# Kernel optimization log

Hardware: AMD Instinct MI355X
Metric: run time of the kernel (lower is better)

The kernel has to match this reference:

```python
import jax, jax.numpy as jnp
import numpy as np

E = 1024
M = 6
GH = 256
FR = 16  # FiLM bottleneck r = max(16, E//64)


def setup_inputs() -> dict:
    key = jax.random.key(0)
    ks = jax.random.split(key, 32)
    n = lambda k, shape, std=0.02: jax.random.normal(k, shape, dtype=jnp.float32) * std
    inp = {
        "x": jax.random.normal(ks[0], (4, 2048, E), dtype=jnp.float32),
        # gate MLP E->GH->M
        "gw1": n(ks[1], (E, GH)), "gb1": jnp.zeros((GH,), jnp.float32),
        "gw2": n(ks[2], (GH, M)), "gb2": jnp.zeros((M,), jnp.float32),
        "ebias": jnp.zeros((M,), jnp.float32),
        "pm_alpha": jnp.float32(0.5),
        # expert 0: DoubleMLP E->2E->E
        "dfc_w": n(ks[3], (E, 2 * E)), "dfc_b": jnp.zeros((2 * E,), jnp.float32),
        "dproj_w": n(ks[4], (2 * E, E)), "dproj_b": jnp.zeros((E,), jnp.float32),
        # expert 1: SingleMLP E->E->E
        "sfc_w": n(ks[5], (E, E)), "sfc_b": jnp.zeros((E,), jnp.float32),
        "sproj_w": n(ks[6], (E, E)), "sproj_b": jnp.zeros((E,), jnp.float32),
        # expert 2: rank-2 perceptron
        "p2_w": n(ks[7], (2, E)), "p2_v": n(ks[8], (2, E)),
        "p2_alpha": jnp.ones((2,), jnp.float32), "p2_b": jnp.zeros((2,), jnp.float32),
        "p2_bias": jnp.zeros((E,), jnp.float32),
        # expert 3: rank-4 perceptron
        "p4_w": n(ks[9], (4, E)), "p4_v": n(ks[10], (4, E)),
        "p4_alpha": jnp.ones((4,), jnp.float32), "p4_b": jnp.zeros((4,), jnp.float32),
        "p4_bias": jnp.zeros((E,), jnp.float32),
        # expert 4: ReGLU1D
        "rg_u": n(ks[11], (E,)), "rg_a": jnp.ones((E,), jnp.float32),
        "rg_b": jnp.zeros((1,), jnp.float32), "rg_bias": jnp.zeros((E,), jnp.float32),
        # expert 5: FiLM E->FR->2E
        "fl_dw": n(ks[12], (E, FR)), "fl_db": jnp.zeros((FR,), jnp.float32),
        "fl_uw": n(ks[13], (FR, 2 * E)), "fl_ub": jnp.zeros((2 * E,), jnp.float32),
    }
    return inp


def _gelu(x):
    return jax.nn.gelu(x, approximate=False)  # torch nn.GELU default (erf)


def _rank_n(x, w, v, alpha, b, biasvec):
    # y = biasvec + sum_i alpha_i * gelu(<w_i,x> + b_i) * v_i
    s = jnp.einsum("bse,ne->bsn", x, w) + b
    g = _gelu(s)
    return jnp.einsum("bsn,ne->bse", alpha * g, v) + biasvec


def reference(x, gw1, gb1, gw2, gb2, ebias, pm_alpha,
              dfc_w, dfc_b, dproj_w, dproj_b,
              sfc_w, sfc_b, sproj_w, sproj_b,
              p2_w, p2_v, p2_alpha, p2_b, p2_bias,
              p4_w, p4_v, p4_alpha, p4_b, p4_bias,
              rg_u, rg_a, rg_b, rg_bias,
              fl_dw, fl_db, fl_uw, fl_ub):
    # gate logits [B,S,M]; tau=1.0
    gl = _gelu(x @ gw1 + gb1) @ gw2 + gb2 + ebias
    pi = jax.nn.softmax(gl, axis=-1)
    # top_k=1 sparse weights: mask to top-1 then renormalize
    _, topi = jax.lax.top_k(pi, 1)
    mask = jax.nn.one_hot(topi[..., 0], M, dtype=pi.dtype)
    w = pi * mask
    w = w / (jnp.sum(w, axis=-1, keepdims=True) + 1e-9)

    # experts (dropout = identity in eval)
    o0 = _gelu(x @ dfc_w + dfc_b) @ dproj_w + dproj_b            # DoubleMLP
    o1 = _gelu(x @ sfc_w + sfc_b) @ sproj_w + sproj_b            # SingleMLP
    o2 = _rank_n(x, p2_w, p2_v, p2_alpha, p2_b, p2_bias)          # perc2
    o3 = _rank_n(x, p4_w, p4_v, p4_alpha, p4_b, p4_bias)          # perc4
    s = x @ rg_u + rg_b[0]                                        # ReGLU1D
    o4 = jax.nn.sigmoid(s)[..., None] * (x * rg_a) + rg_bias
    t = _gelu(x @ fl_dw + fl_db)                                  # FiLM
    gb = t @ fl_uw + fl_ub
    gamma, beta = jnp.split(gb, 2, axis=-1)
    o5 = gamma * x + beta

    all_out = jnp.stack([o0, o1, o2, o3, o4, o5], axis=-1)        # [B,S,E,M]
    mixed = jnp.sum(all_out * w[..., None, :], axis=-1)
    return pm_alpha * mixed
```

## Files before the change

kernel.cpp:

```cpp
#include <hip/hip_runtime.h>
#include <math.h>


#define E 1024
#define GH 256
#define NEXP 6
#define NTOK 8192
#define NCH 24

typedef __attribute__((ext_vector_type(8))) short bf16x8;
typedef __attribute__((ext_vector_type(4))) float f32x4;

__device__ __forceinline__ float gelu_erf(float v) {
    return 0.5f * v * (1.0f + erff(v * 0.70710678118654752440f));
}

__device__ __forceinline__ unsigned short f2bf(float f) {
    union { float f; unsigned u; } c; c.f = f;
    unsigned u = c.u;
    u += 0x7fffu + ((u >> 16) & 1u);
    return (unsigned short)(u >> 16);
}

__device__ __forceinline__ float bf2f(unsigned short h) {
    union { unsigned u; float f; } c; c.u = ((unsigned)h) << 16;
    return c.f;
}

__device__ __forceinline__ int ldso(int row, int q) {
    return row * 32 + ((q ^ ((row >> 1) & 3)) << 3);
}

__device__ __forceinline__ void glds16(const void* g, void* l) {
    __builtin_amdgcn_global_load_lds(
        (const __attribute__((address_space(1))) void*)g,
        (__attribute__((address_space(3))) void*)l, 16, 0, 0);
}

__global__ __launch_bounds__(256)
void prep_kernel(const float* __restrict__ x, unsigned short* __restrict__ xh,
                 unsigned short* __restrict__ xl,
                 const float* __restrict__ gw1, unsigned short* __restrict__ w1cat,
                 const float* __restrict__ p2_w, const float* __restrict__ p4_w,
                 const float* __restrict__ rg_u, const float* __restrict__ fl_dw,
                 unsigned short* __restrict__ w1cheap,
                 const float* __restrict__ dfc_w, unsigned short* __restrict__ dfc_wt,
                 const float* __restrict__ dproj_w, unsigned short* __restrict__ dpj_wt,
                 const float* __restrict__ sfc_w, unsigned short* __restrict__ sfc_wt,
                 const float* __restrict__ sproj_w, unsigned short* __restrict__ spj_wt) {
    __shared__ float tile[32][33];
    const int tid = threadIdx.x;
    const int tx = tid & 31, ty = tid >> 5;
    int b = blockIdx.x;
    if (b < 2048) {
        const int n4 = NTOK * E / 4;
        for (int i = b * 256 + tid; i < n4; i += 2048 * 256) {
            float4 v = reinterpret_cast<const float4*>(x)[i];
            ushort4 h, l;
            h.x = f2bf(v.x); l.x = f2bf(v.x - bf2f(h.x));
            h.y = f2bf(v.y); l.y = f2bf(v.y - bf2f(h.y));
            h.z = f2bf(v.z); l.z = f2bf(v.z - bf2f(h.z));
            h.w = f2bf(v.w); l.w = f2bf(v.w - bf2f(h.w));
            reinterpret_cast<ushort4*>(xh)[i] = h;
            reinterpret_cast<ushort4*>(xl)[i] = l;
        }
        return;
    }
    b -= 2048;
    if (b < 256) {
        const int c0 = (b & 7) * 32, r0 = (b >> 3) * 32;
#pragma unroll
        for (int i = 0; i < 4; ++i)
            tile[ty + i * 8][tx] = gw1[(size_t)(r0 + ty + i * 8) * GH + c0 + tx];
        __syncthreads();
#pragma unroll
        for (int i = 0; i < 4; ++i) {
            float v = tile[tx][ty + i * 8];
            unsigned short h = f2bf(v);
            size_t row = (size_t)(c0 + ty + i * 8) * 2048;
            w1cat[row + r0 + tx] = h;
            w1cat[row + 1024 + r0 + tx] = f2bf(v - bf2f(h));
        }
        return;
    }
    b -= 256;
    if (b < 64) {
        const int r = b;
        const int k4 = tid * 4;
        float4 v = {0.f, 0.f, 0.f, 0.f};
        if (r < 2)       v = *reinterpret_cast<const float4*>(&p2_w[r * E + k4]);
        else if (r < 6)  v = *reinterpret_cast<const float4*>(&p4_w[(r - 2) * E + k4]);
        else if (r == 6) v = *reinterpret_cast<const float4*>(&rg_u[k4]);
        else if (r < 23) {
            const int j = r - 7;
            v.x = fl_dw[(k4 + 0) * 16 + j];
            v.y = fl_dw[(k4 + 1) * 16 + j];
            v.z = fl_dw[(k4 + 2) * 16 + j];
            v.w = fl_dw[(k4 + 3) * 16 + j];
        }
        ushort4 h, l;
        h.x = f2bf(v.x); l.x = f2bf(v.x - bf2f(h.x));
        h.y = f2bf(v.y); l.y = f2bf(v.y - bf2f(h.y));
        h.z = f2bf(v.z); l.z = f2bf(v.z - bf2f(h.z));
        h.w = f2bf(v.w); l.w = f2bf(v.w - bf2f(h.w));
        *reinterpret_cast<ushort4*>(&w1cheap[r * 2048 + k4]) = h;
        *reinterpret_cast<ushort4*>(&w1cheap[r * 2048 + 1024 + k4]) = l;
        return;
    }
    b -= 64;
    const float* src; unsigned short* dst; int R, C, nbx;
    if (b < 2048)      { src = dfc_w;   dst = dfc_wt; R = 1024; C = 2048; nbx = 64; }
    else if (b < 4096) { src = dproj_w; dst = dpj_wt; R = 2048; C = 1024; nbx = 32; b -= 2048; }
    else if (b < 5120) { src = sfc_w;   dst = sfc_wt; R = 1024; C = 1024; nbx = 32; b -= 4096; }
    else               { src = sproj_w; dst = spj_wt; R = 1024; C = 1024; nbx = 32; b -= 5120; }
    const int c0 = (b % nbx) * 32, r0 = (b / nbx) * 32;
#pragma unroll
    for (int i = 0; i < 4; ++i)
        tile[ty + i * 8][tx] = src[(size_t)(r0 + ty + i * 8) * C + c0 + tx];
    __syncthreads();
#pragma unroll
    for (int i = 0; i < 4; ++i)
        dst[(size_t)(c0 + ty + i * 8) * R + r0 + tx] = f2bf(tile[tx][ty + i * 8]);
}

__global__ __launch_bounds__(256)
void gate_partial_kernel(const unsigned short* __restrict__ xh,
                         const unsigned short* __restrict__ xl,
                         const unsigned short* __restrict__ w1cat,
                         const unsigned short* __restrict__ w1cheap,
                         float* __restrict__ hp,
                         float* __restrict__ cdot) {
    __shared__ __align__(16) unsigned short As[2][128 * 64];
    __shared__ __align__(16) unsigned short Bs[2][128 * 64];
    const int tid = threadIdx.x;
    const int bid = blockIdx.x;
    const int xcd = bid & 7, slot = bid >> 3;
    const int nx = slot & 1;
    const int strip = xcd * 32 + (slot >> 1);
    const int m = strip >> 2, c2 = strip & 3;
    const int z = c2 & 1, h = c2 >> 1;
    const int t0 = m * 128, n0 = nx * 128;
    const unsigned short* A = z ? xl : xh;
    float* hpz = hp + (size_t)c2 * ((size_t)NTOK * GH);
    float* cd  = cdot + (size_t)c2 * ((size_t)NTOK * NCH);

    const int lane = tid & 63, wv = tid >> 6;
    const int wr = wv >> 1, wc = wv & 1;
    const int lm = lane & 15, q = lane >> 4;
    const int r0 = tid >> 2, gsl = tid & 3;
    const int g = gsl ^ ((r0 >> 1) & 3);
    const int lbase = wv * 512;

    const unsigned short* pa0 = A + (size_t)(t0 + r0) * E + g * 8;
    const unsigned short* pa1 = A + (size_t)(t0 + 64 + r0) * E + g * 8;
    const unsigned short* pb0 = w1cat + (size_t)(n0 + r0) * 2048 + h * 1024 + g * 8;
    const unsigned short* pb1 = w1cat + (size_t)(n0 + 64 + r0) * 2048 + h * 1024 + g * 8;
    const unsigned short* pcw = w1cheap + (size_t)(nx * 16 + lm) * 2048 + h * 1024 + q * 8;

    f32x4 acc[4][4];
#pragma unroll
    for (int s = 0; s < 4; ++s)
#pragma unroll
        for (int t = 0; t < 4; ++t) acc[s][t] = (f32x4){0.f, 0.f, 0.f, 0.f};
    f32x4 accC[2];
    accC[0] = (f32x4){0.f, 0.f, 0.f, 0.f};
    accC[1] = (f32x4){0.f, 0.f, 0.f, 0.f};

    glds16(pa0, &As[0][lbase]);
    glds16(pa1, &As[0][2048 + lbase]);
    glds16(pa0 + 32, &As[0][4096 + lbase]);
    glds16(pa1 + 32, &As[0][4096 + 2048 + lbase]);
    glds16(pb0, &Bs[0][lbase]);
    glds16(pb1, &Bs[0][2048 + lbase]);
    glds16(pb0 + 32, &Bs[0][4096 + lbase]);
    glds16(pb1 + 32, &Bs[0][4096 + 2048 + lbase]);
    bf16x8 cf0 = *(const bf16x8*)pcw;
    bf16x8 cf1 = *(const bf16x8*)(pcw + 32);

    int cur = 0;
    for (int k0 = 0;; k0 += 64) {
        __syncthreads();
        const int kn = k0 + 64;
        bf16x8 cf0n, cf1n;
        if (kn < 1024) {
            glds16(pa0 + kn, &As[cur ^ 1][lbase]);
            glds16(pa1 + kn, &As[cur ^ 1][2048 + lbase]);
            glds16(pa0 + kn + 32, &As[cur ^ 1][4096 + lbase]);
            glds16(pa1 + kn + 32, &As[cur ^ 1][4096 + 2048 + lbase]);
            glds16(pb0 + kn, &Bs[cur ^ 1][lbase]);
            glds16(pb1 + kn, &Bs[cur ^ 1][2048 + lbase]);
            glds16(pb0 + kn + 32, &Bs[cur ^ 1][4096 + lbase]);
            glds16(pb1 + kn + 32, &Bs[cur ^ 1][4096 + 2048 + lbase]);
            cf0n = *(const bf16x8*)(pcw + kn);
            cf1n = *(const bf16x8*)(pcw + kn + 32);
        }
#pragma unroll
        for (int sub = 0; sub < 2; ++sub) {
            const int off = sub * 4096;
            bf16x8 af[4], bfr[4];
#pragma unroll
            for (int s = 0; s < 4; ++s) af[s] = *(const bf16x8*)&As[cur][off + ldso(wr * 64 + s * 16 + lm, q)];
#pragma unroll
            for (int t = 0; t < 4; ++t) bfr[t] = *(const bf16x8*)&Bs[cur][off + ldso(wc * 64 + t * 16 + lm, q)];
#pragma unroll
            for (int s = 0; s < 4; ++s)
#pragma unroll
                for (int t = 0; t < 4; ++t)
                    acc[s][t] = __builtin_amdgcn_mfma_f32_16x16x32_bf16(af[s], bfr[t], acc[s][t], 0, 0, 0);
            bf16x8 cf = sub ? cf1 : cf0;
            bf16x8 ac0 = wc ? af[2] : af[0];
            bf16x8 ac1 = wc ? af[3] : af[1];
            accC[0] = __builtin_amdgcn_mfma_f32_16x16x32_bf16(ac0, cf, accC[0], 0, 0, 0);
            accC[1] = __builtin_amdgcn_mfma_f32_16x16x32_bf16(ac1, cf, accC[1], 0, 0, 0);
        }
        if (kn >= 1024) break;
        cf0 = cf0n; cf1 = cf1n; cur ^= 1;
    }
#pragma unroll
    for (int s = 0; s < 4; ++s)
#pragma unroll
        for (int t = 0; t < 4; ++t)
#pragma unroll
            for (int rg = 0; rg < 4; ++rg) {
                int rl = wr * 64 + s * 16 + q * 4 + rg;
                int c  = wc * 64 + t * 16 + lm;
                hpz[(size_t)(t0 + rl) * GH + n0 + c] = acc[s][t][rg];
            }
    const int cc = nx * 16 + lm;
    if (cc < NCH) {
#pragma unroll
        for (int i = 0; i < 2; ++i)
#pragma unroll
            for (int rg = 0; rg < 4; ++rg) {
                int rl = wr * 64 + wc * 32 + i * 16 + q * 4 + rg;
                cd[(size_t)(t0 + rl) * NCH + cc] = accC[i][rg];
            }
    }
}

__global__ __launch_bounds__(256)
void gate_finalize_kernel(const float* __restrict__ hp,
                          const float* __restrict__ gb1, const float* __restrict__ gw2,
                          const float* __restrict__ gb2, const float* __restrict__ ebias,
                          const float* __restrict__ pm_alpha,
                          const float* __restrict__ cdot,
                          const float* __restrict__ p2_alpha, const float* __restrict__ p2_b,
                          const float* __restrict__ p4_alpha, const float* __restrict__ p4_b,
                          const float* __restrict__ rg_b, const float* __restrict__ fl_db,
                          float* __restrict__ scale, int* __restrict__ counts,
                          int* __restrict__ tlist, int* __restrict__ eid,
                          float* __restrict__ gvec) {
    __shared__ float hs[32][264];
    __shared__ float g2s[GH * NEXP];
    __shared__ int tokexp[32];
    const int tid = threadIdx.x;
    const int t0 = blockIdx.x * 32;
    const size_t HPS = (size_t)NTOK * GH;
    for (int i = tid; i < GH * NEXP; i += 256) g2s[i] = gw2[i];
#pragma unroll
    for (int i = 0; i < 8; ++i) {
        int f4 = i * 256 + tid;
        int row = f4 >> 6, c4 = (f4 & 63) * 4;
        size_t base = (size_t)(t0 + row) * GH + c4;
        float4 a = *reinterpret_cast<const float4*>(&hp[base]);
        float4 b = *reinterpret_cast<const float4*>(&hp[HPS + base]);
        float4 c = *reinterpret_cast<const float4*>(&hp[2 * HPS + base]);
        float4 d = *reinterpret_cast<const float4*>(&hp[3 * HPS + base]);
        float4 o;
        o.x = gelu_erf(a.x + b.x + c.x + d.x + gb1[c4 + 0]);
        o.y = gelu_erf(a.y + b.y + c.y + d.y + gb1[c4 + 1]);
        o.z = gelu_erf(a.z + b.z + c.z + d.z + gb1[c4 + 2]);
        o.w = gelu_erf(a.w + b.w + c.w + d.w + gb1[c4 + 3]);
        *reinterpret_cast<float4*>(&hs[row][c4]) = o;
    }
    __syncthreads();
    const int t = tid >> 3, j = tid & 7;
    float p[NEXP] = {0.f, 0.f, 0.f, 0.f, 0.f, 0.f};
#pragma unroll 8
    for (int kk = 0; kk < 32; ++kk) {
        int k = j + kk * 8;
        float hv = hs[t][k];
        const float* gr = &g2s[k * NEXP];
#pragma unroll
        for (int m = 0; m < NEXP; ++m) p[m] += hv * gr[m];
    }
#pragma unroll
    for (int m = 0; m < NEXP; ++m) {
        p[m] += __shfl_xor(p[m], 4, 64);
        p[m] += __shfl_xor(p[m], 2, 64);
        p[m] += __shfl_xor(p[m], 1, 64);
    }
    if (j == 0) {
        float L[NEXP];
#pragma unroll
        for (int m = 0; m < NEXP; ++m) L[m] = p[m] + gb2[m] + ebias[m];
        float mx = L[0]; int am = 0;
#pragma unroll
        for (int m = 1; m < NEXP; ++m) { if (L[m] > mx) { mx = L[m]; am = m; } }
        float S = 0.f;
#pragma unroll
        for (int m = 0; m < NEXP; ++m) S += expf(L[m] - mx);
        float pt = 1.f / S;
        scale[t0 + t] = pm_alpha[0] * (pt / (pt + 1e-9f));
        eid[t0 + t] = am;
        tokexp[t] = am;
    }
    __syncthreads();
    if (tid < NEXP) {
        const int e = tid;
        int cnt = 0;
#pragma unroll
        for (int i = 0; i < 32; ++i) cnt += (tokexp[i] == e);
        if (cnt) {
            int base = atomicAdd(&counts[e], cnt);
            int pos = 0;
#pragma unroll
            for (int i = 0; i < 32; ++i)
                if (tokexp[i] == e) tlist[e * NTOK + base + (pos++)] = t0 + i;
        }
    }
    const size_t CDS = (size_t)NTOK * NCH;
    for (int i = tid; i < 32 * NCH; i += 256) {
        const int tt = i / NCH, slot = i - tt * NCH;
        const int tok = t0 + tt;
        size_t idx = (size_t)tok * NCH + slot;
        float s = cdot[idx] + cdot[CDS + idx] + cdot[2 * CDS + idx] + cdot[3 * CDS + idx];
        float val;
        if (slot < 2)       val = p2_alpha[slot] * gelu_erf(s + p2_b[slot]);
        else if (slot < 6)  val = p4_alpha[slot - 2] * gelu_erf(s + p4_b[slot - 2]);
        else if (slot == 6) val = 1.f / (1.f + expf(-(s + rg_b[0])));
        else if (slot < 23) val = gelu_erf(s + fl_db[slot - 7]);
        else                val = 0.f;
        gvec[(size_t)tok * NCH + slot] = val;
    }
}

__global__ __launch_bounds__(256)
void gemm1_cheap_kernel(const unsigned short* __restrict__ xh,
                        const unsigned short* __restrict__ B0, const unsigned short* __restrict__ B1,
                        const float* __restrict__ bias0, const float* __restrict__ bias1,
                        const int* __restrict__ counts, const int* __restrict__ tlist,
                        unsigned short* __restrict__ H0, unsigned short* __restrict__ H1,
                        const float* __restrict__ scale, const float* __restrict__ x,
                        const float* __restrict__ gvec,
                        const float* __restrict__ p2_v, const float* __restrict__ p2_bias,
                        const float* __restrict__ p4_v, const float* __restrict__ p4_bias,
                        const float* __restrict__ rg_a, const float* __restrict__ rg_bias,
                        const float* __restrict__ fl_uw, const float* __restrict__ fl_ub,
                        float* __restrict__ out) {
    __shared__ __align__(16) char smem[2 * 64 * 64 * 2 * 2 + 64 * 4];
    const int tid = threadIdx.x;
    const int bb = blockIdx.x;
    const int lane = tid & 63;

    if (bb < 2048) {
        const int xcd = bb & 7, slot = bb >> 3;
        const int nx = slot & 31;
        const int strip = xcd + 8 * (slot >> 5);
        const int z = strip & 1;
        const int N = z ? 1024 : 2048;
        const int cnt = counts[z];
        const int i0 = (strip >> 1) * 64;
        const int n0 = nx * 64;
        if (i0 >= cnt || n0 >= N) return;
        const unsigned short* Bz = z ? B1 : B0;
        const float* bias = z ? bias1 : bias0;

        unsigned short (*As)[64 * 64] = (unsigned short (*)[64 * 64])smem;
        unsigned short (*Bs)[64 * 64] = (unsigned short (*)[64 * 64])(smem + 2 * 64 * 64 * 2);
        int* toks = (int*)(smem + 2 * 64 * 64 * 2 * 2);
        if (tid < 64) toks[tid] = tlist[z * NTOK + min(i0 + tid, cnt - 1)];
        __syncthreads();

        const int wv = tid >> 6;
        const int wm = (wv & 1) * 32, wn = (wv >> 1) * 32;
        const int lm = lane & 15, q = lane >> 4;
        const int r0 = tid >> 2, gsl = tid & 3;
        const int g = gsl ^ ((r0 >> 1) & 3);
        const int lbase = wv * 512;

        const unsigned short* pa = xh + (size_t)toks[r0] * E + g * 8;
        const unsigned short* pb = Bz + (size_t)(n0 + r0) * E + g * 8;

        f32x4 acc[2][2];
#pragma unroll
        for (int s = 0; s < 2; ++s)
#pragma unroll
            for (int t = 0; t < 2; ++t) acc[s][t] = (f32x4){0.f, 0.f, 0.f, 0.f};

        glds16(pa, &As[0][lbase]);
        glds16(pa + 32, &As[0][2048 + lbase]);
        glds16(pb, &Bs[0][lbase]);
        glds16(pb + 32, &Bs[0][2048 + lbase]);

        int cur = 0;
        for (int k0 = 0;; k0 += 64) {
            __syncthreads();
            const int kn = k0 + 64;
            if (kn < E) {
                glds16(pa + kn, &As[cur ^ 1][lbase]);
                glds16(pa + kn + 32, &As[cur ^ 1][2048 + lbase]);
                glds16(pb + kn, &Bs[cur ^ 1][lbase]);
                glds16(pb + kn + 32, &Bs[cur ^ 1][2048 + lbase]);
            }
#pragma unroll
            for (int sub = 0; sub < 2; ++sub) {
                const int off = sub * 2048;
                bf16x8 af[2], bfr[2];
#pragma unroll
                for (int s = 0; s < 2; ++s) af[s] = *(const bf16x8*)&As[cur][off + ldso(wm + s * 16 + lm, q)];
#pragma unroll
                for (int t = 0; t < 2; ++t) bfr[t] = *(const bf16x8*)&Bs[cur][off + ldso(wn + t * 16 + lm, q)];
#pragma unroll
                for (int s = 0; s < 2; ++s)
#pragma unroll
                    for (int t = 0; t < 2; ++t)
                        acc[s][t] = __builtin_amdgcn_mfma_f32_16x16x32_bf16(af[s], bfr[t], acc[s][t], 0, 0, 0);
            }
            if (kn >= E) break;
            cur ^= 1;
        }
        unsigned short* Hz = z ? H1 : H0;
#pragma unroll
        for (int s = 0; s < 2; ++s)
#pragma unroll
            for (int t = 0; t < 2; ++t)
#pragma unroll
                for (int rg = 0; rg < 4; ++rg) {
                    int rl = wm + s * 16 + q * 4 + rg;
                    int gc = n0 + wn + t * 16 + lm;
                    float v = acc[s][t][rg] + bias[gc];
                    Hz[(size_t)(i0 + rl) * N + gc] = f2bf(gelu_erf(v));
                }
        return;
    }

    int* stoks = (int*)smem;
    float* ssc = (float*)(smem + 32);
    float (*sgv)[17] = (float (*)[17])(smem + 64);
    const int k4 = tid * 4;
    for (int s = bb - 2048; s < 4096; s += 2048) {
        const int e = 2 + (s & 3);
        const int ti = s >> 2;
        const int cnt = counts[e];
        const int i0 = ti * 8;
        if (i0 >= cnt) continue;
        const int nt = min(8, cnt - i0);
        __syncthreads();
        if (tid < 128) {
            const int tt = tid >> 4, sl = tid & 15;
            const int tk = tlist[e * NTOK + min(i0 + tt, cnt - 1)];
            if (sl == 0) { stoks[tt] = tk; ssc[tt] = scale[tk]; }
            const int base = (e == 2) ? 0 : (e == 3) ? 2 : (e == 4) ? 6 : 7;
            const int ng   = (e == 2) ? 2 : (e == 3) ? 4 : (e == 4) ? 1 : 16;
            if (sl < ng) sgv[tt][sl] = gvec[(size_t)tk * NCH + base + sl];
        }
        __syncthreads();
        if (e == 2) {
            const float4 b0 = *reinterpret_cast<const float4*>(&p2_bias[k4]);
            const float4 v0 = *reinterpret_cast<const float4*>(&p2_v[k4]);
            const float4 v1 = *reinterpret_cast<const float4*>(&p2_v[E + k4]);
#pragma unroll
            for (int tt = 0; tt < 8; ++tt) {
                if (tt < nt) {
                    const float g0 = sgv[tt][0], g1 = sgv[tt][1], sc = ssc[tt];
                    float4 o;
                    o.x = (b0.x + g0 * v0.x + g1 * v1.x) * sc;
                    o.y = (b0.y + g0 * v0.y + g1 * v1.y) * sc;
                    o.z = (b0.z + g0 * v0.z + g1 * v1.z) * sc;
                    o.w = (b0.w + g0 * v0.w + g1 * v1.w) * sc;
                    *reinterpret_cast<float4*>(&out[(size_t)stoks[tt] * E + k4]) = o;
                }
            }
        } else if (e == 3) {
            const float4 b0 = *reinterpret_cast<const float4*>(&p4_bias[k4]);
            float4 vv[4];
#pragma unroll
            for (int j = 0; j < 4; ++j)
                vv[j] = *reinterpret_cast<const float4*>(&p4_v[j * E + k4]);
#pragma unroll
            for (int tt = 0; tt < 8; ++tt) {
                if (tt < nt) {
                    float4 o = b0;
#pragma unroll
                    for (int j = 0; j < 4; ++j) {
                        const float gj = sgv[tt][j];
                        o.x += gj * vv[j].x; o.y += gj * vv[j].y;
                        o.z += gj * vv[j].z; o.w += gj * vv[j].w;
                    }
                    const float sc = ssc[tt];
                    o.x *= sc; o.y *= sc; o.z *= sc; o.w *= sc;
                    *reinterpret_cast<float4*>(&out[(size_t)stoks[tt] * E + k4]) = o;
                }
            }
        } else if (e == 4) {
            const float4 av = *reinterpret_cast<const float4*>(&rg_a[k4]);
            const float4 bv = *reinterpret_cast<const float4*>(&rg_bias[k4]);
#pragma unroll
            for (int tt = 0; tt < 8; ++tt) {
                if (tt < nt) {
                    const float sg = sgv[tt][0], sc = ssc[tt];
                    const float4 xv = *reinterpret_cast<const float4*>(&x[(size_t)stoks[tt] * E + k4]);
                    float4 o;
                    o.x = (sg * xv.x * av.x + bv.x) * sc;
                    o.y = (sg * xv.y * av.y + bv.y) * sc;
                    o.z = (sg * xv.z * av.z + bv.z) * sc;
                    o.w = (sg * xv.w * av.w + bv.w) * sc;
                    *reinterpret_cast<float4*>(&out[(size_t)stoks[tt] * E + k4]) = o;
                }
            }
        } else {
#pragma unroll
            for (int half = 0; half < 2; ++half) {
                float4 ga[4], be[4];
                const float4 g0 = *reinterpret_cast<const float4*>(&fl_ub[k4]);
                const float4 b0 = *reinterpret_cast<const float4*>(&fl_ub[E + k4]);
#pragma unroll
                for (int tt = 0; tt < 4; ++tt) { ga[tt] = g0; be[tt] = b0; }
#pragma unroll
                for (int j = 0; j < 16; ++j) {
                    const float4 ug = *reinterpret_cast<const float4*>(&fl_uw[(size_t)j * 2 * E + k4]);
                    const float4 ub = *reinterpret_cast<const float4*>(&fl_uw[(size_t)j * 2 * E + E + k4]);
#pragma unroll
                    for (int tt = 0; tt < 4; ++tt) {
                        const float tj = sgv[half * 4 + tt][j];
                        ga[tt].x += tj * ug.x; ga[tt].y += tj * ug.y;
                        ga[tt].z += tj * ug.z; ga[tt].w += tj * ug.w;
                        be[tt].x += tj * ub.x; be[tt].y += tj * ub.y;
                        be[tt].z += tj * ub.z; be[tt].w += tj * ub.w;
                    }
                }
#pragma unroll
                for (int tt = 0; tt < 4; ++tt) {
                    const int ix = half * 4 + tt;
                    if (ix < nt) {
                        const float sc = ssc[ix];
                        const float4 xv = *reinterpret_cast<const float4*>(&x[(size_t)stoks[ix] * E + k4]);
                        float4 o;
                        o.x = (ga[tt].x * xv.x + be[tt].x) * sc;
                        o.y = (ga[tt].y * xv.y + be[tt].y) * sc;
                        o.z = (ga[tt].z * xv.z + be[tt].z) * sc;
                        o.w = (ga[tt].w * xv.w + be[tt].w) * sc;
                        *reinterpret_cast<float4*>(&out[(size_t)stoks[ix] * E + k4]) = o;
                    }
                }
            }
        }
    }
}

__global__ __launch_bounds__(256)
void moe_gemm2_kernel(const unsigned short* __restrict__ h1, const unsigned short* __restrict__ h2,
                      const unsigned short* __restrict__ dpj, const unsigned short* __restrict__ spj,
                      const float* __restrict__ dproj_b, const float* __restrict__ sproj_b,
                      const int* __restrict__ counts, const int* __restrict__ tlist,
                      const float* __restrict__ scale,
                      float* __restrict__ out) {
    __shared__ __align__(16) unsigned short As[2][64 * 64];
    __shared__ __align__(16) unsigned short Bs[2][64 * 64];
    __shared__ int toks[64];
    const int tid = threadIdx.x;
    const int bb = blockIdx.x;
    const int lane = tid & 63;

    const int xcd = bb & 7, slot = bb >> 3;
    const int nx = slot & 15;
    const int strip = xcd + 8 * (slot >> 4);
    const int z = strip & 1;
    const int i0 = (strip >> 1) * 64;
    const int n0 = nx * 64;
    const int K = z ? 1024 : 2048;
    const int cnt = counts[z];
    if (i0 >= cnt) return;
    const int rows = min(64, cnt - i0);
    const unsigned short* Az = z ? h2 : h1;
    const unsigned short* Bz = z ? spj : dpj;
    const float* bias = z ? sproj_b : dproj_b;

    if (tid < 64) toks[tid] = tlist[z * NTOK + min(i0 + tid, cnt - 1)];
    __syncthreads();

    const int wv = tid >> 6;
    const int wm = (wv & 1) * 32, wn = (wv >> 1) * 32;
    const int lm = lane & 15, q = lane >> 4;
    const int r0 = tid >> 2, gsl = tid & 3;
    const int g = gsl ^ ((r0 >> 1) & 3);
    const int lbase = wv * 512;

    const unsigned short* pa = Az + (size_t)(i0 + r0) * K + g * 8;
    const unsigned short* pb = Bz + (size_t)(n0 + r0) * K + g * 8;

    f32x4 acc[2][2];
#pragma unroll
    for (int s = 0; s < 2; ++s)
#pragma unroll
        for (int t = 0; t < 2; ++t) acc[s][t] = (f32x4){0.f, 0.f, 0.f, 0.f};

    glds16(pa, &As[0][lbase]);
    glds16(pa + 32, &As[0][2048 + lbase]);
    glds16(pb, &Bs[0][lbase]);
    glds16(pb + 32, &Bs[0][2048 + lbase]);

    int cur = 0;
    for (int k0 = 0;; k0 += 64) {
        __syncthreads();
        const int kn = k0 + 64;
        if (kn < K) {
            glds16(pa + kn, &As[cur ^ 1][lbase]);
            glds16(pa + kn + 32, &As[cur ^ 1][2048 + lbase]);
            glds16(pb + kn, &Bs[cur ^ 1][lbase]);
            glds16(pb + kn + 32, &Bs[cur ^ 1][2048 + lbase]);
        }
#pragma unroll
        for (int sub = 0; sub < 2; ++sub) {
            const int off = sub * 2048;
            bf16x8 af[2], bfr[2];
#pragma unroll
            for (int s = 0; s < 2; ++s) af[s] = *(const bf16x8*)&As[cur][off + ldso(wm + s * 16 + lm, q)];
#pragma unroll
            for (int t = 0; t < 2; ++t) bfr[t] = *(const bf16x8*)&Bs[cur][off + ldso(wn + t * 16 + lm, q)];
#pragma unroll
            for (int s = 0; s < 2; ++s)
#pragma unroll
                for (int t = 0; t < 2; ++t)
                    acc[s][t] = __builtin_amdgcn_mfma_f32_16x16x32_bf16(af[s], bfr[t], acc[s][t], 0, 0, 0);
        }
        if (kn >= K) break;
        cur ^= 1;
    }
#pragma unroll
    for (int s = 0; s < 2; ++s)
#pragma unroll
        for (int t = 0; t < 2; ++t)
#pragma unroll
            for (int rg = 0; rg < 4; ++rg) {
                int rl = wm + s * 16 + q * 4 + rg;
                if (rl < rows) {
                    int gc = n0 + wn + t * 16 + lm;
                    int tok = toks[rl];
                    out[(size_t)tok * E + gc] = scale[tok] * (acc[s][t][rg] + bias[gc]);
                }
            }
}

extern "C" void kernel_launch(void* const* d_in, const int* in_sizes, int n_in,
                              void* d_out, int out_size, void* d_ws, size_t ws_size,
                              hipStream_t stream) {
    const float* x        = (const float*)d_in[0];
    const float* gw1      = (const float*)d_in[1];
    const float* gb1      = (const float*)d_in[2];
    const float* gw2      = (const float*)d_in[3];
    const float* gb2      = (const float*)d_in[4];
    const float* ebias    = (const float*)d_in[5];
    const float* pm_alpha = (const float*)d_in[6];
    const float* dfc_w    = (const float*)d_in[7];
    const float* dfc_b    = (const float*)d_in[8];
    const float* dproj_w  = (const float*)d_in[9];
    const float* dproj_b  = (const float*)d_in[10];
    const float* sfc_w    = (const float*)d_in[11];
    const float* sfc_b    = (const float*)d_in[12];
    const float* sproj_w  = (const float*)d_in[13];
    const float* sproj_b  = (const float*)d_in[14];
    const float* p2_w     = (const float*)d_in[15];
    const float* p2_v     = (const float*)d_in[16];
    const float* p2_alpha = (const float*)d_in[17];
    const float* p2_b     = (const float*)d_in[18];
    const float* p2_bias  = (const float*)d_in[19];
    const float* p4_w     = (const float*)d_in[20];
    const float* p4_v     = (const float*)d_in[21];
    const float* p4_alpha = (const float*)d_in[22];
    const float* p4_b     = (const float*)d_in[23];
    const float* p4_bias  = (const float*)d_in[24];
    const float* rg_u     = (const float*)d_in[25];
    const float* rg_a     = (const float*)d_in[26];
    const float* rg_b     = (const float*)d_in[27];
    const float* rg_bias  = (const float*)d_in[28];
    const float* fl_dw    = (const float*)d_in[29];
    const float* fl_db    = (const float*)d_in[30];
    const float* fl_uw    = (const float*)d_in[31];
    const float* fl_ub    = (const float*)d_in[32];
    float* out = (float*)d_out;

    char* ws = (char*)d_ws;
    size_t off = 0;
    int*            counts = (int*)(ws + off);            off += 256;
    float*          scale  = (float*)(ws + off);          off += (size_t)NTOK * 4;
    int*            tlist  = (int*)(ws + off);            off += (size_t)NEXP * NTOK * 4;
    int*            eid    = (int*)(ws + off);            off += (size_t)NTOK * 4;
    float*          gvec   = (float*)(ws + off);          off += (size_t)NTOK * NCH * 4;
    float*          cdot   = (float*)(ws + off);          off += (size_t)4 * NTOK * NCH * 4;
    unsigned short* w1cheap= (unsigned short*)(ws + off); off += (size_t)64 * 2048 * 2;
    unsigned short* w1cat  = (unsigned short*)(ws + off); off += (size_t)GH * 2048 * 2;
    unsigned short* dfc_wt = (unsigned short*)(ws + off); off += (size_t)2048 * 1024 * 2;
    unsigned short* dpj_wt = (unsigned short*)(ws + off); off += (size_t)1024 * 2048 * 2;
    unsigned short* sfc_wt = (unsigned short*)(ws + off); off += (size_t)1024 * 1024 * 2;
    unsigned short* spj_wt = (unsigned short*)(ws + off); off += (size_t)1024 * 1024 * 2;
    unsigned short* x_hi   = (unsigned short*)(ws + off); off += (size_t)NTOK * E * 2;
    char* U = ws + off;
    unsigned short* x_lo = (unsigned short*)U;
    unsigned short* h1   = (unsigned short*)U;
    unsigned short* h2   = (unsigned short*)(U + (size_t)16 * 1024 * 1024);
    float* hp = out;

    hipMemsetAsync(counts, 0, 256, stream);
    prep_kernel<<<8512, 256, 0, stream>>>(x, x_hi, x_lo, gw1, w1cat,
                                          p2_w, p4_w, rg_u, fl_dw, w1cheap,
                                          dfc_w, dfc_wt, dproj_w, dpj_wt,
                                          sfc_w, sfc_wt, sproj_w, spj_wt);
    gate_partial_kernel<<<512, 256, 0, stream>>>(
        x_hi, x_lo, w1cat, w1cheap, hp, cdot);
    gate_finalize_kernel<<<NTOK / 32, 256, 0, stream>>>(
        hp, gb1, gw2, gb2, ebias, pm_alpha, cdot,
        p2_alpha, p2_b, p4_alpha, p4_b, rg_b, fl_db,
        scale, counts, tlist, eid, gvec);
    gemm1_cheap_kernel<<<4096, 256, 0, stream>>>(
        x_hi, dfc_wt, sfc_wt, dfc_b, sfc_b, counts, tlist, h1, h2,
        scale, x, gvec,
        p2_v, p2_bias, p4_v, p4_bias,
        rg_a, rg_bias, fl_uw, fl_ub, out);
    moe_gemm2_kernel<<<1024, 256, 0, stream>>>(
        h1, h2, dpj_wt, spj_wt, dproj_b, sproj_b, counts, tlist, scale, out);
    (void)in_sizes; (void)n_in; (void)out_size; (void)ws_size;
}
```

Measured before the change: 291.1 us.

## Triple-buffer MoE GEMM loads and split cheap experts into separate kernel

Both expert GEMM kernels move from double to triple-buffered LDS staging. They use explicit vmcnt waits and raw barriers so two tiles stay in flight ahead of the MFMA compute. The fused gemm1+cheap-expert kernel is split into a dedicated GEMM1 kernel and a standalone cheap_kernel launched after GEMM2. The FiLM path now handles all 8 tokens in one pass instead of two halves of 4. The split costs one extra launch and gives up overlap of the cheap experts with GEMM1, in exchange for simpler GEMM blocks. The 8-token FiLM pass holds more accumulators per thread, which raises register pressure.

```diff
diff --git a/kernel.cpp b/kernel.cpp
--- a/kernel.cpp
+++ b/kernel.cpp
@@ -335,111 +335,201 @@
     }
 }
 
+#define STAGEAB(t, jb)                                            \
+    do {                                                          \
+        glds16(pa + (t) * 64,      &As[jb][lbase]);               \
+        glds16(pa + (t) * 64 + 32, &As[jb][2048 + lbase]);        \
+        glds16(pb + (t) * 64,      &Bs[jb][lbase]);               \
+        glds16(pb + (t) * 64 + 32, &Bs[jb][2048 + lbase]);        \
+    } while (0)
+
 __global__ __launch_bounds__(256)
-void gemm1_cheap_kernel(const unsigned short* __restrict__ xh,
-                        const unsigned short* __restrict__ B0, const unsigned short* __restrict__ B1,
-                        const float* __restrict__ bias0, const float* __restrict__ bias1,
-                        const int* __restrict__ counts, const int* __restrict__ tlist,
-                        unsigned short* __restrict__ H0, unsigned short* __restrict__ H1,
-                        const float* __restrict__ scale, const float* __restrict__ x,
-                        const float* __restrict__ gvec,
-                        const float* __restrict__ p2_v, const float* __restrict__ p2_bias,
-                        const float* __restrict__ p4_v, const float* __restrict__ p4_bias,
-                        const float* __restrict__ rg_a, const float* __restrict__ rg_bias,
-                        const float* __restrict__ fl_uw, const float* __restrict__ fl_ub,
-                        float* __restrict__ out) {
-    __shared__ __align__(16) char smem[2 * 64 * 64 * 2 * 2 + 64 * 4];
+void moe_gemm1_kernel(const unsigned short* __restrict__ xh,
+                      const unsigned short* __restrict__ B0, const unsigned short* __restrict__ B1,
+                      const float* __restrict__ bias0, const float* __restrict__ bias1,
+                      const int* __restrict__ counts, const int* __restrict__ tlist,
+                      unsigned short* __restrict__ H0, unsigned short* __restrict__ H1) {
+    __shared__ __align__(16) unsigned short As[3][64 * 64];
+    __shared__ __align__(16) unsigned short Bs[3][64 * 64];
+    __shared__ int toks[64];
+    const int tid = threadIdx.x;
+    const int bid = blockIdx.x;
+    const int xcd = bid & 7, slot = bid >> 3;
+    const int nx = slot & 31;
+    const int strip = xcd + 8 * (slot >> 5);
+    const int z = strip & 1;
+    const int N = z ? 1024 : 2048;
+    const int cnt = counts[z];
+    const int i0 = (strip >> 1) * 64;
+    const int n0 = nx * 64;
+    if (i0 >= cnt || n0 >= N) return;
+    const unsigned short* Bz = z ? B1 : B0;
+    const float* bias = z ? bias1 : bias0;
+
+    if (tid < 64) toks[tid] = tlist[z * NTOK + min(i0 + tid, cnt - 1)];
+    __syncthreads();
+
+    const int lane = tid & 63, wv = tid >> 6;
+    const int wm = (wv & 1) * 32, wn = (wv >> 1) * 32;
+    const int lm = lane & 15, q = lane >> 4;
+    const int r0 = tid >> 2, gsl = tid & 3;
+    const int g = gsl ^ ((r0 >> 1) & 3);
+    const int lbase = wv * 512;
+
+    const unsigned short* pa = xh + (size_t)toks[r0] * E + g * 8;
+    const unsigned short* pb = Bz + (size_t)(n0 + r0) * E + g * 8;
+
+    f32x4 acc[2][2];
+#pragma unroll
+    for (int s = 0; s < 2; ++s)
+#pragma unroll
+        for (int t = 0; t < 2; ++t) acc[s][t] = (f32x4){0.f, 0.f, 0.f, 0.f};
+
+    STAGEAB(0, 0); STAGEAB(1, 1); STAGEAB(2, 2);
+
+    const int nt = E / 64;
+    for (int i = 0; i < nt; ++i) {
+        const int ahead = nt - 1 - i;
+        if (ahead >= 2)      asm volatile("s_waitcnt vmcnt(8)" ::: "memory");
+        else if (ahead == 1) asm volatile("s_waitcnt vmcnt(4)" ::: "memory");
+        else                 asm volatile("s_waitcnt vmcnt(0)" ::: "memory");
+        asm volatile("s_barrier" ::: "memory");
+        const int jb = i % 3;
+#pragma unroll
+        for (int sub = 0; sub < 2; ++sub) {
+            const int off = sub * 2048;
+            bf16x8 af[2], bfr[2];
+#pragma unroll
+            for (int s = 0; s < 2; ++s) af[s] = *(const bf16x8*)&As[jb][off + ldso(wm + s * 16 + lm, q)];
+#pragma unroll
+            for (int t = 0; t < 2; ++t) bfr[t] = *(const bf16x8*)&Bs[jb][off + ldso(wn + t * 16 + lm, q)];
+#pragma unroll
+            for (int s = 0; s < 2; ++s)
+#pragma unroll
+                for (int t = 0; t < 2; ++t)
+                    acc[s][t] = __builtin_amdgcn_mfma_f32_16x16x32_bf16(af[s], bfr[t], acc[s][t], 0, 0, 0);
+        }
+        asm volatile("s_barrier" ::: "memory");
+        if (i + 3 < nt) STAGEAB(i + 3, jb);
+    }
+    unsigned short* Hz = z ? H1 : H0;
+#pragma unroll
+    for (int s = 0; s < 2; ++s)
+#pragma unroll
+        for (int t = 0; t < 2; ++t)
+#pragma unroll
+            for (int rg = 0; rg < 4; ++rg) {
+                int rl = wm + s * 16 + q * 4 + rg;
+                int gc = n0 + wn + t * 16 + lm;
+                float v = acc[s][t][rg] + bias[gc];
+                Hz[(size_t)(i0 + rl) * N + gc] = f2bf(gelu_erf(v));
+            }
+}
+
+__global__ __launch_bounds__(256)
+void moe_gemm2_kernel(const unsigned short* __restrict__ h1, const unsigned short* __restrict__ h2,
+                      const unsigned short* __restrict__ dpj, const unsigned short* __restrict__ spj,
+                      const float* __restrict__ dproj_b, const float* __restrict__ sproj_b,
+                      const int* __restrict__ counts, const int* __restrict__ tlist,
+                      const float* __restrict__ scale,
+                      float* __restrict__ out) {
+    __shared__ __align__(16) unsigned short As[3][64 * 64];
+    __shared__ __align__(16) unsigned short Bs[3][64 * 64];
+    __shared__ int toks[64];
     const int tid = threadIdx.x;
     const int bb = blockIdx.x;
     const int lane = tid & 63;
 
-    if (bb < 2048) {
-        const int xcd = bb & 7, slot = bb >> 3;
-        const int nx = slot & 31;
-        const int strip = xcd + 8 * (slot >> 5);
-        const int z = strip & 1;
-        const int N = z ? 1024 : 2048;
-        const int cnt = counts[z];
-        const int i0 = (strip >> 1) * 64;
-        const int n0 = nx * 64;
-        if (i0 >= cnt || n0 >= N) return;
-        const unsigned short* Bz = z ? B1 : B0;
-        const float* bias = z ? bias1 : bias0;
-
-        unsigned short (*As)[64 * 64] = (unsigned short (*)[64 * 64])smem;
-        unsigned short (*Bs)[64 * 64] = (unsigned short (*)[64 * 64])(smem + 2 * 64 * 64 * 2);
-        int* toks = (int*)(smem + 2 * 64 * 64 * 2 * 2);
-        if (tid < 64) toks[tid] = tlist[z * NTOK + min(i0 + tid, cnt - 1)];
-        __syncthreads();
-
-        const int wv = tid >> 6;
-        const int wm = (wv & 1) * 32, wn = (wv >> 1) * 32;
-        const int lm = lane & 15, q = lane >> 4;
-        const int r0 = tid >> 2, gsl = tid & 3;
-        const int g = gsl ^ ((r0 >> 1) & 3);
-        const int lbase = wv * 512;
-
-        const unsigned short* pa = xh + (size_t)toks[r0] * E + g * 8;
-        const unsigned short* pb = Bz + (size_t)(n0 + r0) * E + g * 8;
-
-        f32x4 acc[2][2];
-#pragma unroll
-        for (int s = 0; s < 2; ++s)
-#pragma unroll
-            for (int t = 0; t < 2; ++t) acc[s][t] = (f32x4){0.f, 0.f, 0.f, 0.f};
-
-        glds16(pa, &As[0][lbase]);
-        glds16(pa + 32, &As[0][2048 + lbase]);
-        glds16(pb, &Bs[0][lbase]);
-        glds16(pb + 32, &Bs[0][2048 + lbase]);
-
-        int cur = 0;
-        for (int k0 = 0;; k0 += 64) {
-            __syncthreads();
-            const int kn = k0 + 64;
-            if (kn < E) {
-                glds16(pa + kn, &As[cur ^ 1][lbase]);
-                glds16(pa + kn + 32, &As[cur ^ 1][2048 + lbase]);
-                glds16(pb + kn, &Bs[cur ^ 1][lbase]);
-                glds16(pb + kn + 32, &Bs[cur ^ 1][2048 + lbase]);
-            }
-#pragma unroll
-            for (int sub = 0; sub < 2; ++sub) {
-                const int off = sub * 2048;
-                bf16x8 af[2], bfr[2];
-#pragma unroll
-                for (int s = 0; s < 2; ++s) af[s] = *(const bf16x8*)&As[cur][off + ldso(wm + s * 16 + lm, q)];
-#pragma unroll
-                for (int t = 0; t < 2; ++t) bfr[t] = *(const bf16x8*)&Bs[cur][off + ldso(wn + t * 16 + lm, q)];
-#pragma unroll
-                for (int s = 0; s < 2; ++s)
-#pragma unroll
-                    for (int t = 0; t < 2; ++t)
-                        acc[s][t] = __builtin_amdgcn_mfma_f32_16x16x32_bf16(af[s], bfr[t], acc[s][t], 0, 0, 0);
-            }
-            if (kn >= E) break;
-            cur ^= 1;
-        }
-        unsigned short* Hz = z ? H1 : H0;
-#pragma unroll
-        for (int s = 0; s < 2; ++s)
-#pragma unroll
-            for (int t = 0; t < 2; ++t)
-#pragma unroll
-                for (int rg = 0; rg < 4; ++rg) {
-                    int rl = wm + s * 16 + q * 4 + rg;
+    const int xcd = bb & 7, slot = bb >> 3;
+    const int nx = slot & 15;
+    const int strip = xcd + 8 * (slot >> 4);
+    const int z = strip & 1;
+    const int i0 = (strip >> 1) * 64;
+    const int n0 = nx * 64;
+    const int K = z ? 1024 : 2048;
+    const int cnt = counts[z];
+    if (i0 >= cnt) return;
+    const int rows = min(64, cnt - i0);
+    const unsigned short* Az = z ? h2 : h1;
+    const unsigned short* Bz = z ? spj : dpj;
+    const float* bias = z ? sproj_b : dproj_b;
+
+    if (tid < 64) toks[tid] = tlist[z * NTOK + min(i0 + tid, cnt - 1)];
+    __syncthreads();
+
+    const int wv = tid >> 6;
+    const int wm = (wv & 1) * 32, wn = (wv >> 1) * 32;
+    const int lm = lane & 15, q = lane >> 4;
+    const int r0 = tid >> 2, gsl = tid & 3;
+    const int g = gsl ^ ((r0 >> 1) & 3);
+    const int lbase = wv * 512;
+
+    const unsigned short* pa = Az + (size_t)(i0 + r0) * K + g * 8;
+    const unsigned short* pb = Bz + (size_t)(n0 + r0) * K + g * 8;
+
+    f32x4 acc[2][2];
+#pragma unroll
+    for (int s = 0; s < 2; ++s)
+#pragma unroll
+        for (int t = 0; t < 2; ++t) acc[s][t] = (f32x4){0.f, 0.f, 0.f, 0.f};
+
+    STAGEAB(0, 0); STAGEAB(1, 1); STAGEAB(2, 2);
+
+    const int nt = K / 64;
+    for (int i = 0; i < nt; ++i) {
+        const int ahead = nt - 1 - i;
+        if (ahead >= 2)      asm volatile("s_waitcnt vmcnt(8)" ::: "memory");
+        else if (ahead == 1) asm volatile("s_waitcnt vmcnt(4)" ::: "memory");
+        else                 asm volatile("s_waitcnt vmcnt(0)" ::: "memory");
+        asm volatile("s_barrier" ::: "memory");
+        const int jb = i % 3;
+#pragma unroll
+        for (int sub = 0; sub < 2; ++sub) {
+            const int off = sub * 2048;
+            bf16x8 af[2], bfr[2];
+#pragma unroll
+            for (int s = 0; s < 2; ++s) af[s] = *(const bf16x8*)&As[jb][off + ldso(wm + s * 16 + lm, q)];
+#pragma unroll
+            for (int t = 0; t < 2; ++t) bfr[t] = *(const bf16x8*)&Bs[jb][off + ldso(wn + t * 16 + lm, q)];
+#pragma unroll
+            for (int s = 0; s < 2; ++s)
+#pragma unroll
+                for (int t = 0; t < 2; ++t)
+                    acc[s][t] = __builtin_amdgcn_mfma_f32_16x16x32_bf16(af[s], bfr[t], acc[s][t], 0, 0, 0);
+        }
+        asm volatile("s_barrier" ::: "memory");
+        if (i + 3 < nt) STAGEAB(i + 3, jb);
+    }
+#pragma unroll
+    for (int s = 0; s < 2; ++s)
+#pragma unroll
+        for (int t = 0; t < 2; ++t)
+#pragma unroll
+            for (int rg = 0; rg < 4; ++rg) {
+                int rl = wm + s * 16 + q * 4 + rg;
+                if (rl < rows) {
                     int gc = n0 + wn + t * 16 + lm;
-                    float v = acc[s][t][rg] + bias[gc];
-                    Hz[(size_t)(i0 + rl) * N + gc] = f2bf(gelu_erf(v));
+                    int tok = toks[rl];
+                    out[(size_t)tok * E + gc] = scale[tok] * (acc[s][t][rg] + bias[gc]);
                 }
-        return;
-    }
-
-    int* stoks = (int*)smem;
-    float* ssc = (float*)(smem + 32);
-    float (*sgv)[17] = (float (*)[17])(smem + 64);
+            }
+}
+
+__global__ __launch_bounds__(256)
+void cheap_kernel(const int* __restrict__ counts, const int* __restrict__ tlist,
+                  const float* __restrict__ scale, const float* __restrict__ x,
+                  const float* __restrict__ gvec,
+                  const float* __restrict__ p2_v, const float* __restrict__ p2_bias,
+                  const float* __restrict__ p4_v, const float* __restrict__ p4_bias,
+                  const float* __restrict__ rg_a, const float* __restrict__ rg_bias,
+                  const float* __restrict__ fl_uw, const float* __restrict__ fl_ub,
+                  float* __restrict__ out) {
+    __shared__ int stoks[8];
+    __shared__ float ssc[8];
+    __shared__ float sgv[8][17];
+    const int tid = threadIdx.x;
     const int k4 = tid * 4;
-    for (int s = bb - 2048; s < 4096; s += 2048) {
+    for (int s = blockIdx.x; s < 4096; s += 2048) {
         const int e = 2 + (s & 3);
         const int ti = s >> 2;
         const int cnt = counts[e];
@@ -510,137 +600,39 @@
                 }
             }
         } else {
-#pragma unroll
-            for (int half = 0; half < 2; ++half) {
-                float4 ga[4], be[4];
-                const float4 g0 = *reinterpret_cast<const float4*>(&fl_ub[k4]);
-                const float4 b0 = *reinterpret_cast<const float4*>(&fl_ub[E + k4]);
-#pragma unroll
-                for (int tt = 0; tt < 4; ++tt) { ga[tt] = g0; be[tt] = b0; }
-#pragma unroll
-                for (int j = 0; j < 16; ++j) {
-                    const float4 ug = *reinterpret_cast<const float4*>(&fl_uw[(size_t)j * 2 * E + k4]);
-                    const float4 ub = *reinterpret_cast<const float4*>(&fl_uw[(size_t)j * 2 * E + E + k4]);
-#pragma unroll
-                    for (int tt = 0; tt < 4; ++tt) {
-                        const float tj = sgv[half * 4 + tt][j];
-                        ga[tt].x += tj * ug.x; ga[tt].y += tj * ug.y;
-                        ga[tt].z += tj * ug.z; ga[tt].w += tj * ug.w;
-                        be[tt].x += tj * ub.x; be[tt].y += tj * ub.y;
-                        be[tt].z += tj * ub.z; be[tt].w += tj * ub.w;
-                    }
+            float4 ga[8], be[8];
+            const float4 g0 = *reinterpret_cast<const float4*>(&fl_ub[k4]);
+            const float4 b0 = *reinterpret_cast<const float4*>(&fl_ub[E + k4]);
+#pragma unroll
+            for (int tt = 0; tt < 8; ++tt) { ga[tt] = g0; be[tt] = b0; }
+#pragma unroll
+            for (int j = 0; j < 16; ++j) {
+                const float4 ug = *reinterpret_cast<const float4*>(&fl_uw[(size_t)j * 2 * E + k4]);
+                const float4 ub = *reinterpret_cast<const float4*>(&fl_uw[(size_t)j * 2 * E + E + k4]);
+#pragma unroll
+                for (int tt = 0; tt < 8; ++tt) {
+                    const float tj = sgv[tt][j];
+                    ga[tt].x += tj * ug.x; ga[tt].y += tj * ug.y;
+                    ga[tt].z += tj * ug.z; ga[tt].w += tj * ug.w;
+                    be[tt].x += tj * ub.x; be[tt].y += tj * ub.y;
+                    be[tt].z += tj * ub.z; be[tt].w += tj * ub.w;
                 }
-#pragma unroll
-                for (int tt = 0; tt < 4; ++tt) {
-                    const int ix = half * 4 + tt;
-                    if (ix < nt) {
-                        const float sc = ssc[ix];
-                        const float4 xv = *reinterpret_cast<const float4*>(&x[(size_t)stoks[ix] * E + k4]);
-                        float4 o;
-                        o.x = (ga[tt].x * xv.x + be[tt].x) * sc;
-                        o.y = (ga[tt].y * xv.y + be[tt].y) * sc;
-                        o.z = (ga[tt].z * xv.z + be[tt].z) * sc;
-                        o.w = (ga[tt].w * xv.w + be[tt].w) * sc;
-                        *reinterpret_cast<float4*>(&out[(size_t)stoks[ix] * E + k4]) = o;
-                    }
+            }
+#pragma unroll
+            for (int tt = 0; tt < 8; ++tt) {
+                if (tt < nt) {
+                    const float sc = ssc[tt];
+                    const float4 xv = *reinterpret_cast<const float4*>(&x[(size_t)stoks[tt] * E + k4]);
+                    float4 o;
+                    o.x = (ga[tt].x * xv.x + be[tt].x) * sc;
+                    o.y = (ga[tt].y * xv.y + be[tt].y) * sc;
+                    o.z = (ga[tt].z * xv.z + be[tt].z) * sc;
+                    o.w = (ga[tt].w * xv.w + be[tt].w) * sc;
+                    *reinterpret_cast<float4*>(&out[(size_t)stoks[tt] * E + k4]) = o;
                 }
             }
         }
     }
-}
-
-__global__ __launch_bounds__(256)
-void moe_gemm2_kernel(const unsigned short* __restrict__ h1, const unsigned short* __restrict__ h2,
-                      const unsigned short* __restrict__ dpj, const unsigned short* __restrict__ spj,
-                      const float* __restrict__ dproj_b, const float* __restrict__ sproj_b,
-                      const int* __restrict__ counts, const int* __restrict__ tlist,
-                      const float* __restrict__ scale,
-                      float* __restrict__ out) {
-    __shared__ __align__(16) unsigned short As[2][64 * 64];
-    __shared__ __align__(16) unsigned short Bs[2][64 * 64];
-    __shared__ int toks[64];
-    const int tid = threadIdx.x;
-    const int bb = blockIdx.x;
-    const int lane = tid & 63;
-
-    const int xcd = bb & 7, slot = bb >> 3;
-    const int nx = slot & 15;
-    const int strip = xcd + 8 * (slot >> 4);
-    const int z = strip & 1;
-    const int i0 = (strip >> 1) * 64;
-    const int n0 = nx * 64;
-    const int K = z ? 1024 : 2048;
-    const int cnt = counts[z];
-    if (i0 >= cnt) return;
-    const int rows = min(64, cnt - i0);
-    const unsigned short* Az = z ? h2 : h1;
-    const unsigned short* Bz = z ? spj : dpj;
-    const float* bias = z ? sproj_b : dproj_b;
-
-    if (tid < 64) toks[tid] = tlist[z * NTOK + min(i0 + tid, cnt - 1)];
-    __syncthreads();
-
-    const int wv = tid >> 6;
-    const int wm = (wv & 1) * 32, wn = (wv >> 1) * 32;
-    const int lm = lane & 15, q = lane >> 4;
-    const int r0 = tid >> 2, gsl = tid & 3;
-    const int g = gsl ^ ((r0 >> 1) & 3);
-    const int lbase = wv * 512;
-
-    const unsigned short* pa = Az + (size_t)(i0 + r0) * K + g * 8;
-    const unsigned short* pb = Bz + (size_t)(n0 + r0) * K + g * 8;
-
-    f32x4 acc[2][2];
-#pragma unroll
-    for (int s = 0; s < 2; ++s)
-#pragma unroll
-        for (int t = 0; t < 2; ++t) acc[s][t] = (f32x4){0.f, 0.f, 0.f, 0.f};
-
-    glds16(pa, &As[0][lbase]);
-    glds16(pa + 32, &As[0][2048 + lbase]);
-    glds16(pb, &Bs[0][lbase]);
-    glds16(pb + 32, &Bs[0][2048 + lbase]);
-
-    int cur = 0;
-    for (int k0 = 0;; k0 += 64) {
-        __syncthreads();
-        const int kn = k0 + 64;
-        if (kn < K) {
-            glds16(pa + kn, &As[cur ^ 1][lbase]);
-            glds16(pa + kn + 32, &As[cur ^ 1][2048 + lbase]);
-            glds16(pb + kn, &Bs[cur ^ 1][lbase]);
-            glds16(pb + kn + 32, &Bs[cur ^ 1][2048 + lbase]);
-        }
-#pragma unroll
-        for (int sub = 0; sub < 2; ++sub) {
-            const int off = sub * 2048;
-            bf16x8 af[2], bfr[2];
-#pragma unroll
-            for (int s = 0; s < 2; ++s) af[s] = *(const bf16x8*)&As[cur][off + ldso(wm + s * 16 + lm, q)];
-#pragma unroll
-            for (int t = 0; t < 2; ++t) bfr[t] = *(const bf16x8*)&Bs[cur][off + ldso(wn + t * 16 + lm, q)];
-#pragma unroll
-            for (int s = 0; s < 2; ++s)
-#pragma unroll
-                for (int t = 0; t < 2; ++t)
-                    acc[s][t] = __builtin_amdgcn_mfma_f32_16x16x32_bf16(af[s], bfr[t], acc[s][t], 0, 0, 0);
-        }
-        if (kn >= K) break;
-        cur ^= 1;
-    }
-#pragma unroll
-    for (int s = 0; s < 2; ++s)
-#pragma unroll
-        for (int t = 0; t < 2; ++t)
-#pragma unroll
-            for (int rg = 0; rg < 4; ++rg) {
-                int rl = wm + s * 16 + q * 4 + rg;
-                if (rl < rows) {
-                    int gc = n0 + wn + t * 16 + lm;
-                    int tok = toks[rl];
-                    out[(size_t)tok * E + gc] = scale[tok] * (acc[s][t][rg] + bias[gc]);
-                }
-            }
 }
 
 extern "C" void kernel_launch(void* const* d_in, const int* in_sizes, int n_in,
@@ -713,12 +705,13 @@
         hp, gb1, gw2, gb2, ebias, pm_alpha, cdot,
         p2_alpha, p2_b, p4_alpha, p4_b, rg_b, fl_db,
         scale, counts, tlist, eid, gvec);
-    gemm1_cheap_kernel<<<4096, 256, 0, stream>>>(
-        x_hi, dfc_wt, sfc_wt, dfc_b, sfc_b, counts, tlist, h1, h2,
-        scale, x, gvec,
+    moe_gemm1_kernel<<<2048, 256, 0, stream>>>(
+        x_hi, dfc_wt, sfc_wt, dfc_b, sfc_b, counts, tlist, h1, h2);
+    moe_gemm2_kernel<<<1024, 256, 0, stream>>>(
+        h1, h2, dpj_wt, spj_wt, dproj_b, sproj_b, counts, tlist, scale, out);
+    cheap_kernel<<<2048, 256, 0, stream>>>(
+        counts, tlist, scale, x, gvec,
         p2_v, p2_bias, p4_v, p4_bias,
         rg_a, rg_bias, fl_uw, fl_ub, out);
-    moe_gemm2_kernel<<<1024, 256, 0, stream>>>(
-        h1, h2, dpj_wt, spj_wt, dproj_b, sproj_b, counts, tlist, scale, out);
     (void)in_sizes; (void)n_in; (void)out_size; (void)ws_size;
 }
```

Result: faster. 283.6 us (-2.6%).
